# Optimization experiments

Measured on AMD Instinct MI355X. Metric: run time of the kernel, lower is better.

Reference implementation:

```python
import jax, jax.numpy as jnp
import numpy as np

DIM = 2048
N_HEADS = 16
Q_LORA = 1536
KV_LORA = 512
NOPE = 128
ROPE = 64
QK_HD = NOPE + ROPE  # 192
V_HD = 128
BS, SEQ = 2, 2048
EPS = 1e-6


def rmsnorm(x, w):
    var = jnp.mean(jnp.square(x), axis=-1, keepdims=True)
    return x * jax.lax.rsqrt(var + EPS) * w


def rope_cos_sin(seq_len, dim, dtype):
    inv_freq = 1.0 / (10000.0 ** (jnp.arange(0, dim, 2, dtype=jnp.float32) / dim))
    t = jnp.arange(seq_len, dtype=jnp.float32)
    freqs = jnp.outer(t, inv_freq)            # [S, dim/2]
    emb = jnp.concatenate([freqs, freqs], -1)  # [S, dim]
    return jnp.cos(emb).astype(dtype), jnp.sin(emb).astype(dtype)


def rotate_half(x):
    x1, x2 = jnp.split(x, 2, axis=-1)
    return jnp.concatenate([-x2, x1], axis=-1)


def apply_rope(x, cos, sin):
    # x: [B, S, H, D]; cos/sin: [S, D] -> broadcast over B, H
    return x * cos[None, :, None, :] + rotate_half(x) * sin[None, :, None, :]


def setup_inputs() -> dict:
    key = jax.random.key(0)
    ks = jax.random.split(key, 8)
    s = 0.02
    return {
        "x": jax.random.normal(ks[0], (BS, SEQ, DIM), jnp.float32),
        "wq_a_w": jax.random.normal(ks[1], (Q_LORA, DIM), jnp.float32) * s,
        "wq_a_b": jnp.zeros((Q_LORA,), jnp.float32),
        "q_norm_w": jnp.ones((Q_LORA,), jnp.float32),
        "wq_b_w": jax.random.normal(ks[2], (N_HEADS * QK_HD, Q_LORA), jnp.float32) * s,
        "wq_b_b": jnp.zeros((N_HEADS * QK_HD,), jnp.float32),
        "wkv_a_w": jax.random.normal(ks[3], (KV_LORA + ROPE, DIM), jnp.float32) * s,
        "wkv_a_b": jnp.zeros((KV_LORA + ROPE,), jnp.float32),
        "kv_norm_w": jnp.ones((KV_LORA,), jnp.float32),
        "wkv_b_w": jax.random.normal(ks[4], (N_HEADS * (NOPE + V_HD), KV_LORA), jnp.float32) * s,
        "wkv_b_b": jnp.zeros((N_HEADS * (NOPE + V_HD),), jnp.float32),
        "wo_w": jax.random.normal(ks[5], (DIM, N_HEADS * V_HD), jnp.float32) * s,
        "wo_b": jnp.zeros((DIM,), jnp.float32),
    }


def reference(x, wq_a_w, wq_a_b, q_norm_w, wq_b_w, wq_b_b,
              wkv_a_w, wkv_a_b, kv_norm_w, wkv_b_w, wkv_b_b, wo_w, wo_b):
    bs, seq_len, _ = x.shape
    # Q path: low-rank down, RMSNorm, up
    q = x @ wq_a_w.T + wq_a_b
    q = rmsnorm(q, q_norm_w)
    q = q @ wq_b_w.T + wq_b_b
    q = q.reshape(bs, seq_len, N_HEADS, QK_HD)
    q_nope, q_pe = q[..., :NOPE], q[..., NOPE:]
    # KV path: joint low-rank + decoupled rope key
    kv = x @ wkv_a_w.T + wkv_a_b
    kv_c, k_pe = kv[..., :KV_LORA], kv[..., KV_LORA:]
    k_pe = k_pe[:, :, None, :]  # [B, S, 1, ROPE]
    cos, sin = rope_cos_sin(seq_len, ROPE, x.dtype)
    q_pe = apply_rope(q_pe, cos, sin)
    k_pe = apply_rope(k_pe, cos, sin)
    # naive mode: materialize per-head K/V
    kv_c = rmsnorm(kv_c, kv_norm_w)
    kvb = (kv_c @ wkv_b_w.T + wkv_b_b).reshape(bs, seq_len, N_HEADS, NOPE + V_HD)
    k_nope, v = kvb[..., :NOPE], kvb[..., NOPE:]
    q_full = jnp.concatenate([q_nope, q_pe], axis=-1)            # [B,S,H,192]
    k_full = jnp.concatenate(
        [k_nope, jnp.broadcast_to(k_pe, (bs, seq_len, N_HEADS, ROPE))], axis=-1)
    scale = 1.0 / np.sqrt(QK_HD)
    scores = jnp.einsum('bqhd,bkhd->bhqk', q_full, k_full) * scale
    causal = jnp.tril(jnp.ones((seq_len, seq_len), bool))
    scores = jnp.where(causal[None, None], scores, jnp.finfo(scores.dtype).min)
    attn = jax.nn.softmax(scores, axis=-1)
    out = jnp.einsum('bhqk,bkhd->bqhd', attn, v)
    out = out.reshape(bs, seq_len, N_HEADS * V_HD)
    return out @ wo_w.T + wo_b
```

## Files before the change

kernel.cpp:

```cpp
#include <hip/hip_runtime.h>

#define SEQ 2048
#define NHEADS 16

typedef __bf16 bf16;
typedef __bf16 bf16x8 __attribute__((ext_vector_type(8)));
typedef __bf16 bf16x4v __attribute__((ext_vector_type(4)));
typedef float f32x4 __attribute__((ext_vector_type(4)));
typedef unsigned short u16x4 __attribute__((ext_vector_type(4)));
typedef unsigned short u16x8 __attribute__((ext_vector_type(8)));

static __device__ __forceinline__ float bf2f(unsigned short u) {
    union { unsigned u32; float f; } v; v.u32 = ((unsigned)u) << 16; return v.f;
}
static __device__ __forceinline__ unsigned short f2bf(float f) {
    union { float f; unsigned u; } v; v.f = f;
    unsigned u = v.u;
    unsigned r = u + 0x7fffu + ((u >> 16) & 1u);
    return (unsigned short)(r >> 16);
}

static __device__ __forceinline__ void g2l16(const unsigned short* g, unsigned short* l) {
    __builtin_amdgcn_global_load_lds(
        (const __attribute__((address_space(1))) unsigned int*)(unsigned long long)g,
        (__attribute__((address_space(3))) unsigned int*)(unsigned int)(unsigned long long)l,
        16, 0, 0);
}

__global__ void detect_dtype(const unsigned* __restrict__ qnw, int* __restrict__ flag) {
    if (threadIdx.x == 0 && blockIdx.x == 0)
        *flag = (qnw[0] == 0x3F800000u) ? 1 : 0;
}

struct CvtArgs {
    const void* src[13];
    unsigned short* dst[13];
    int n[13];
    int startblk[14];
};
__global__ __launch_bounds__(256) void to_bf16_all(CvtArgs a, const int* __restrict__ flag) {
    int bx = blockIdx.x;
    int t = 0;
    while (bx >= a.startblk[t + 1]) ++t;
    int base = (bx - a.startblk[t]) * 4096;
    int n = a.n[t];
    int hi = base + 4096; if (hi > n) hi = n;
    int cnt = hi - base;
    if (*flag) {
        const f32x4* s = (const f32x4*)a.src[t] + (base >> 2);
        u16x4* d = (u16x4*)(a.dst[t] + base);
        int c4 = cnt >> 2;
        for (int e = threadIdx.x; e < c4; e += 256) {
            f32x4 v = s[e];
            u16x4 o;
#pragma unroll
            for (int j = 0; j < 4; ++j) o[j] = f2bf(v[j]);
            d[e] = o;
        }
    } else {
        const uint4* s = (const uint4*)a.src[t] + (base >> 3);
        uint4* d = (uint4*)(a.dst[t] + base);
        int c8 = cnt >> 3;
        for (int e = threadIdx.x; e < c8; e += 256) d[e] = s[e];
    }
}

struct GemmP {
    const unsigned short* A; int lda;
    const unsigned short* W;
    const unsigned short* bias;
    unsigned short* C; float* Cf; int ldc;
    int N; int K; const int* flagp;
    int nbx;
    float oscale;
};

static __device__ void gemm_body(const GemmP g, int bx, int by,
                                 unsigned short* Al, unsigned short* Bl)
{
    const int lane = threadIdx.x & 63;
    const int w    = threadIdx.x >> 6;
    const int r    = lane & 15;
    const int quad = lane >> 4;
    const int m0 = by << 7;
    const int n0 = bx << 7;
    const int wr = (w >> 1) << 6;
    const int wc = (w & 1) << 6;

    const int srow = lane >> 2;
    const int scol = (lane & 3) << 3;
    const int j0 = w * 2, j1 = w * 2 + 1;

    const unsigned short* a0 = g.A + (size_t)(m0 + j0 * 16 + srow) * g.lda + scol;
    const unsigned short* a1 = g.A + (size_t)(m0 + j1 * 16 + srow) * g.lda + scol;
    int bn0 = n0 + j0 * 16 + srow; if (bn0 >= g.N) bn0 = g.N - 1;
    int bn1 = n0 + j1 * 16 + srow; if (bn1 >= g.N) bn1 = g.N - 1;
    const unsigned short* b0 = g.W + (size_t)bn0 * g.K + scol;
    const unsigned short* b1 = g.W + (size_t)bn1 * g.K + scol;

    f32x4 acc[4][4];
#pragma unroll
    for (int mt = 0; mt < 4; ++mt)
#pragma unroll
        for (int nt = 0; nt < 4; ++nt) acc[mt][nt] = (f32x4){0.f, 0.f, 0.f, 0.f};

    auto stage = [&](int buf, int kb) {
        unsigned short* Ad = Al + (buf << 12);
        unsigned short* Bd = Bl + (buf << 12);
        g2l16(a0 + kb, &Ad[j0 * 512 + lane * 8]);
        g2l16(a1 + kb, &Ad[j1 * 512 + lane * 8]);
        g2l16(b0 + kb, &Bd[j0 * 512 + lane * 8]);
        g2l16(b1 + kb, &Bd[j1 * 512 + lane * 8]);
    };

    stage(0, 0);
    __syncthreads();
    int cur = 0;
    for (int kb = 0; kb < g.K; kb += 32) {
        if (kb + 32 < g.K) stage(cur ^ 1, kb + 32);

        const unsigned short* As = Al + (cur << 12);
        const unsigned short* Bs = Bl + (cur << 12);
        bf16x8 af[4], bfr[4];
#pragma unroll
        for (int mt = 0; mt < 4; ++mt)
            af[mt] = *(const bf16x8*)&As[(wr + mt * 16 + r) * 32 + quad * 8];
#pragma unroll
        for (int nt = 0; nt < 4; ++nt)
            bfr[nt] = *(const bf16x8*)&Bs[(wc + nt * 16 + r) * 32 + quad * 8];
#pragma unroll
        for (int mt = 0; mt < 4; ++mt)
#pragma unroll
            for (int nt = 0; nt < 4; ++nt)
                acc[mt][nt] = __builtin_amdgcn_mfma_f32_16x16x32_bf16(af[mt], bfr[nt], acc[mt][nt], 0, 0, 0);

        __syncthreads();
        cur ^= 1;
    }

    int outf = (g.Cf && g.flagp) ? *g.flagp : 0;
    float bv[4];
#pragma unroll
    for (int nt = 0; nt < 4; ++nt) {
        int col = n0 + wc + nt * 16 + r;
        bv[nt] = (g.bias && col < g.N) ? bf2f(g.bias[col]) : 0.f;
    }
#pragma unroll
    for (int mt = 0; mt < 4; ++mt) {
#pragma unroll
        for (int i = 0; i < 4; ++i) {
            int row = m0 + wr + mt * 16 + quad * 4 + i;
#pragma unroll
            for (int nt = 0; nt < 4; ++nt) {
                int col = n0 + wc + nt * 16 + r;
                if (col < g.N) {
                    float v = (acc[mt][nt][i] + bv[nt]) * g.oscale;
                    size_t idx = (size_t)row * g.ldc + col;
                    if (g.Cf) {
                        if (outf) g.Cf[idx] = v;
                        else      ((unsigned short*)g.Cf)[idx] = f2bf(v);
                    } else {
                        g.C[idx] = f2bf(v);
                    }
                }
            }
        }
    }
}

__global__ __launch_bounds__(256) void gemm_one(GemmP g) {
    __shared__ unsigned short Al[2 * 4096];
    __shared__ unsigned short Bl[2 * 4096];
    gemm_body(g, blockIdx.x, blockIdx.y, Al, Bl);
}

__global__ __launch_bounds__(256) void gemm_two(GemmP g0, GemmP g1, int nblk0) {
    __shared__ unsigned short Al[2 * 4096];
    __shared__ unsigned short Bl[2 * 4096];
    int id = blockIdx.x;
    if (id < nblk0) {
        gemm_body(g0, id % g0.nbx, id / g0.nbx, Al, Bl);
    } else {
        id -= nblk0;
        gemm_body(g1, id % g1.nbx, id / g1.nbx, Al, Bl);
    }
}

__global__ __launch_bounds__(256) void rmsnorm_ip2(
    unsigned short* __restrict__ d0, int s0w, int w0w, const unsigned short* __restrict__ w0,
    unsigned short* __restrict__ d1, int s1w, int w1w, const unsigned short* __restrict__ w1,
    int rows0)
{
    __shared__ float red[256];
    int row = blockIdx.x;
    unsigned short* p; const unsigned short* wt; int stride, width;
    if (row < rows0) { p = d0; wt = w0; stride = s0w; width = w0w; }
    else { row -= rows0; p = d1; wt = w1; stride = s1w; width = w1w; }
    p += (size_t)row * stride;

    const int nv = width >> 3;
    u16x8* pv = (u16x8*)p;
    const u16x8* wv = (const u16x8*)wt;

    float ss = 0.f;
    for (int j = threadIdx.x; j < nv; j += 256) {
        u16x8 v = pv[j];
#pragma unroll
        for (int k = 0; k < 8; ++k) { float f = bf2f(v[k]); ss += f * f; }
    }
    red[threadIdx.x] = ss;
    __syncthreads();
    for (int s = 128; s > 0; s >>= 1) {
        if ((int)threadIdx.x < s) red[threadIdx.x] += red[threadIdx.x + s];
        __syncthreads();
    }
    float rstd = rsqrtf(red[0] / (float)width + 1e-6f);
    for (int j = threadIdx.x; j < nv; j += 256) {
        u16x8 v = pv[j], g = wv[j], o;
#pragma unroll
        for (int k = 0; k < 8; ++k) o[k] = f2bf(bf2f(v[k]) * rstd * bf2f(g[k]));
        pv[j] = o;
    }
}

__global__ __launch_bounds__(256) void rope_ip_all(
    unsigned short* __restrict__ qbuf, unsigned short* __restrict__ kvbf)
{
    __shared__ float cst[32], snt[32];
    int row = blockIdx.x;
    int s = row & (SEQ - 1);
    if (threadIdx.x < 32) {
        int i = threadIdx.x;
        float inv = exp2f(-(float)i * (13.2877123795f / 32.0f));
        float ang = (float)s * inv;
        cst[i] = cosf(ang); snt[i] = sinf(ang);
    }
    __syncthreads();
    for (int t = threadIdx.x; t < 544; t += 256) {
        int i = t & 31;
        float c = cst[i], sn = snt[i];
        unsigned short* p;
        if (t < 512) p = qbuf + (size_t)row * 3072 + (t >> 5) * 192 + 128;
        else         p = kvbf + (size_t)row * 576 + 512;
        float x1 = bf2f(p[i]), x2 = bf2f(p[i + 32]);
        p[i]      = f2bf(x1 * c - x2 * sn);
        p[i + 32] = f2bf(x2 * c + x1 * sn);
    }
}

__global__ __launch_bounds__(256) void mla_attn_mfma(
    const unsigned short* __restrict__ qbuf,
    const unsigned short* __restrict__ kvb,
    const unsigned short* __restrict__ kvbuf,
    unsigned short* __restrict__ attn_out)
{
    __shared__ unsigned short Kt[2][32 * 200];
    __shared__ unsigned short Vt[2][128 * 40];
    __shared__ unsigned short Pm[4][16 * 40];

    const int id    = blockIdx.x;
    const int bh    = (id & 7) + (((id >> 3) & 3) << 3);
    const int qtblk = id >> 5;
    const int b = bh >> 4, h = bh & 15;
    const int tid  = threadIdx.x;
    const int lane = tid & 63;
    const int w    = tid >> 6;
    const int r    = lane & 15;
    const int quad = lane >> 4;
    const int rowk0 = b * SEQ;

    int kldso[3];
    const unsigned short* ksrc[3];
    int krst[3];
#pragma unroll
    for (int j = 0; j < 3; ++j) {
        int v = tid + j * 256;
        int row = v / 24, c = v % 24;
        kldso[j] = row * 200 + c * 8;
        if (c < 16) { ksrc[j] = kvb + (size_t)(rowk0 + row) * 4096 + h * 256 + c * 8; krst[j] = 4096; }
        else        { ksrc[j] = kvbuf + (size_t)(rowk0 + row) * 576 + 512 + (c - 16) * 8; krst[j] = 576; }
    }
    const int vp  = tid & 15;
    const int vdc = tid >> 4;
    const unsigned short* vsrc = kvb + (size_t)(rowk0 + 2 * vp) * 4096 + h * 256 + 128 + vdc * 8;

    auto stageK = [&](int buf, const uint4& k0, const uint4& k1, const uint4& k2) {
        *(uint4*)&Kt[buf][kldso[0]] = k0;
        *(uint4*)&Kt[buf][kldso[1]] = k1;
        *(uint4*)&Kt[buf][kldso[2]] = k2;
    };
    auto stageV = [&](int buf, const uint4& va, const uint4& vb_) {
        const unsigned* ea = (const unsigned*)&va;
        const unsigned* eb = (const unsigned*)&vb_;
        unsigned short* Vd = &Vt[buf][0];
#pragma unroll
        for (int t = 0; t < 4; ++t) {
            unsigned pe = (ea[t] & 0xffffu) | (eb[t] << 16);
            unsigned po = (ea[t] >> 16) | (eb[t] & 0xffff0000u);
            *(unsigned*)&Vd[(vdc * 8 + 2 * t) * 40 + 2 * vp]     = pe;
            *(unsigned*)&Vd[(vdc * 8 + 2 * t + 1) * 40 + 2 * vp] = po;
        }
    };

    unsigned short* Pw = Pm[w];

#pragma unroll 1
    for (int half = 0; half < 2; ++half) {
        const int qt = half ? (31 - qtblk) : qtblk;
        const int qbase = qt * 64 + w * 16;
        const int nkb = 2 * qt + 2;
        const int itmax = 2 * qt + (w >> 1);

        bf16x8 qf[6];
        {
            const unsigned short* qp =
                qbuf + (size_t)(rowk0 + qbase + r) * 3072 + h * 192 + quad * 8;
#pragma unroll
            for (int t = 0; t < 6; ++t) qf[t] = *(const bf16x8*)(qp + t * 32);
        }

        f32x4 O[8];
#pragma unroll
        for (int f = 0; f < 8; ++f) O[f] = (f32x4){0.f, 0.f, 0.f, 0.f};
        float mi = -1e30f, li = 0.f;

        uint4 pk0, pk1, pk2, pv0, pv1;

        __syncthreads();
        pk0 = *(const uint4*)(ksrc[0]);
        pk1 = *(const uint4*)(ksrc[1]);
        pk2 = *(const uint4*)(ksrc[2]);
        pv0 = *(const uint4*)(vsrc);
        pv1 = *(const uint4*)(vsrc + 4096);
        stageK(0, pk0, pk1, pk2);
        stageV(0, pv0, pv1);
        __syncthreads();

#pragma unroll 1
        for (int it = 0; it < nkb; ++it) {
            const int p = it & 1;
            const int kb = it * 32;
            const bool more = (it + 1 < nkb);

            if (more) {
                const size_t koff = (size_t)(kb + 32);
                pk0 = *(const uint4*)(ksrc[0] + koff * krst[0]);
                pk1 = *(const uint4*)(ksrc[1] + koff * krst[1]);
                pk2 = *(const uint4*)(ksrc[2] + koff * krst[2]);
                pv0 = *(const uint4*)(vsrc + koff * 4096);
                pv1 = *(const uint4*)(vsrc + koff * 4096 + 4096);
            }

            if (it <= itmax) {
                f32x4 s0 = {0.f, 0.f, 0.f, 0.f}, s1 = {0.f, 0.f, 0.f, 0.f};
                __builtin_amdgcn_s_setprio(1);
#pragma unroll
                for (int t = 0; t < 6; ++t) {
                    bf16x8 k0 = *(const bf16x8*)&Kt[p][r * 200 + t * 32 + quad * 8];
                    bf16x8 k1 = *(const bf16x8*)&Kt[p][(16 + r) * 200 + t * 32 + quad * 8];
                    s0 = __builtin_amdgcn_mfma_f32_16x16x32_bf16(k0, qf[t], s0, 0, 0, 0);
                    s1 = __builtin_amdgcn_mfma_f32_16x16x32_bf16(k1, qf[t], s1, 0, 0, 0);
                }
                __builtin_amdgcn_s_setprio(0);

                const int qrow = qbase + r;
                float a0[4], a1[4];
                float mx = -1e30f;
                if (kb + 31 > qbase) {
#pragma unroll
                    for (int i = 0; i < 4; ++i) {
                        a0[i] = (kb + quad * 4 + i      <= qrow) ? s0[i] : -1e30f;
                        a1[i] = (kb + 16 + quad * 4 + i <= qrow) ? s1[i] : -1e30f;
                        mx = fmaxf(mx, fmaxf(a0[i], a1[i]));
                    }
                } else {
#pragma unroll
                    for (int i = 0; i < 4; ++i) {
                        a0[i] = s0[i];
                        a1[i] = s1[i];
                        mx = fmaxf(mx, fmaxf(a0[i], a1[i]));
                    }
                }
                mx = fmaxf(mx, __shfl_xor(mx, 16, 64));
                mx = fmaxf(mx, __shfl_xor(mx, 32, 64));

                if (!__all(mx <= mi + 8.f)) {
                    float mn = fmaxf(mi, mx);
                    float al = __builtin_amdgcn_exp2f(mi - mn);
#pragma unroll
                    for (int f = 0; f < 8; ++f) O[f] *= al;
                    li *= al;
                    mi = mn;
                }

                float p0[4], p1[4], ps = 0.f;
#pragma unroll
                for (int i = 0; i < 4; ++i) {
                    p0[i] = __builtin_amdgcn_exp2f(a0[i] - mi);
                    p1[i] = __builtin_amdgcn_exp2f(a1[i] - mi);
                    ps += p0[i] + p1[i];
                }
                ps += __shfl_xor(ps, 16, 64);
                ps += __shfl_xor(ps, 32, 64);
                li += ps;

                bf16x4v b0v, b1v;
#pragma unroll
                for (int i = 0; i < 4; ++i) {
                    b0v[i] = (__bf16)p0[i];
                    b1v[i] = (__bf16)p1[i];
                }
                *(bf16x4v*)&Pw[r * 40 + quad * 4]      = b0v;
                *(bf16x4v*)&Pw[r * 40 + 16 + quad * 4] = b1v;

                bf16x8 pf = *(const bf16x8*)&Pw[r * 40 + quad * 8];
                __builtin_amdgcn_s_setprio(1);
#pragma unroll
                for (int f = 0; f < 8; ++f) {
                    bf16x8 vb = *(const bf16x8*)&Vt[p][(f * 16 + r) * 40 + quad * 8];
                    O[f] = __builtin_amdgcn_mfma_f32_16x16x32_bf16(vb, pf, O[f], 0, 0, 0);
                }
                __builtin_amdgcn_s_setprio(0);
            }

            if (more) {
                const int q2 = 1 - p;
                stageK(q2, pk0, pk1, pk2);
                stageV(q2, pv0, pv1);
                __syncthreads();
            }
        }

        float inv = (li > 0.f) ? (1.f / li) : 0.f;
        unsigned short* orow = attn_out + (size_t)(rowk0 + qbase + r) * 2048 + h * 128;
#pragma unroll
        for (int f = 0; f < 8; ++f) {
            bf16x4v o;
#pragma unroll
            for (int i = 0; i < 4; ++i) o[i] = (__bf16)(O[f][i] * inv);
            *(bf16x4v*)&orow[f * 16 + quad * 4] = o;
        }
    }
}

extern "C" void kernel_launch(void* const* d_in, const int* in_sizes, int n_in,
                              void* d_out, int out_size, void* d_ws, size_t ws_size,
                              hipStream_t stream)
{
    char* ws = (char*)d_ws;
    size_t off = 0;
    auto alloc = [&](size_t bytes) -> void* {
        void* p = ws + off;
        off = (off + bytes + 255) & ~(size_t)255;
        return p;
    };

    int* flag = (int*)alloc(256);

    const int nx = 4096 * 2048;
    unsigned short* xb    = (unsigned short*)alloc((size_t)nx * 2);
    unsigned short* wqa   = (unsigned short*)alloc((size_t)1536 * 2048 * 2);
    unsigned short* wqab  = (unsigned short*)alloc(1536 * 2);
    unsigned short* qnw   = (unsigned short*)alloc(1536 * 2);
    unsigned short* wqb   = (unsigned short*)alloc((size_t)3072 * 1536 * 2);
    unsigned short* wqbb  = (unsigned short*)alloc(3072 * 2);
    unsigned short* wkva  = (unsigned short*)alloc((size_t)576 * 2048 * 2);
    unsigned short* wkvab = (unsigned short*)alloc(576 * 2);
    unsigned short* kvnw  = (unsigned short*)alloc(512 * 2);
    unsigned short* wkvb  = (unsigned short*)alloc((size_t)4096 * 512 * 2);
    unsigned short* wkvbb = (unsigned short*)alloc(4096 * 2);
    unsigned short* wo    = (unsigned short*)alloc((size_t)2048 * 2048 * 2);
    unsigned short* wob   = (unsigned short*)alloc(2048 * 2);

    unsigned short* qa   = (unsigned short*)alloc((size_t)4096 * 1536 * 2);
    unsigned short* qbuf = (unsigned short*)alloc((size_t)4096 * 3072 * 2);
    unsigned short* kvbf = (unsigned short*)alloc((size_t)4096 * 576 * 2);
    unsigned short* kvb  = (unsigned short*)alloc((size_t)4096 * 4096 * 2);
    unsigned short* attn = xb;

    const int M = 4096;
    dim3 blk(256);

    detect_dtype<<<dim3(1), dim3(64), 0, stream>>>((const unsigned*)d_in[3], flag);

    {
        CvtArgs a;
        unsigned short* dsts[13] = {xb, wqa, wqab, qnw, wqb, wqbb, wkva, wkvab, kvnw, wkvb, wkvbb, wo, wob};
        int pb = 0;
        for (int i = 0; i < 13; ++i) {
            a.src[i] = d_in[i];
            a.dst[i] = dsts[i];
            a.n[i] = in_sizes[i];
            a.startblk[i] = pb;
            pb += (in_sizes[i] + 4095) / 4096;
        }
        a.startblk[13] = pb;
        to_bf16_all<<<dim3(pb), blk, 0, stream>>>(a, flag);
    }

    auto mkg = [](const unsigned short* A, int lda, const unsigned short* W,
                  const unsigned short* bias, unsigned short* C, float* Cf, int ldc,
                  int N, int K, const int* fl, float osc) -> GemmP {
        GemmP g;
        g.A = A; g.lda = lda; g.W = W; g.bias = bias;
        g.C = C; g.Cf = Cf; g.ldc = ldc; g.N = N; g.K = K; g.flagp = fl;
        g.nbx = (N + 127) / 128;
        g.oscale = osc;
        return g;
    };

    {
        GemmP gqa  = mkg(xb, 2048, wqa,  wqab,  qa,   nullptr, 1536, 1536, 2048, nullptr, 1.f);
        GemmP gkva = mkg(xb, 2048, wkva, wkvab, kvbf, nullptr, 576,  576,  2048, nullptr, 1.f);
        int nb0 = gqa.nbx * (M / 128), nb1 = gkva.nbx * (M / 128);
        gemm_two<<<dim3(nb0 + nb1), blk, 0, stream>>>(gqa, gkva, nb0);
    }

    rmsnorm_ip2<<<dim3(2 * M), blk, 0, stream>>>(qa, 1536, 1536, qnw,
                                                 kvbf, 576, 512, kvnw, M);

    {
        GemmP gqb  = mkg(qa,   1536, wqb,  wqbb,  qbuf, nullptr, 3072, 3072, 1536, nullptr, 0.1041175648f);
        GemmP gkvb = mkg(kvbf, 576,  wkvb, wkvbb, kvb,  nullptr, 4096, 4096, 512,  nullptr, 1.f);
        int nb0 = gqb.nbx * (M / 128), nb1 = gkvb.nbx * (M / 128);
        gemm_two<<<dim3(nb0 + nb1), blk, 0, stream>>>(gqb, gkvb, nb0);
    }

    rope_ip_all<<<dim3(M), blk, 0, stream>>>(qbuf, kvbf);

    mla_attn_mfma<<<dim3(512), blk, 0, stream>>>(qbuf, kvb, kvbf, attn);

    {
        GemmP gout = mkg(attn, 2048, wo, wob, nullptr, (float*)d_out, 2048, 2048, 2048, flag, 1.f);
        gemm_one<<<dim3(gout.nbx, M / 128), blk, 0, stream>>>(gout);
    }
}
```

Baseline: 447.0 us.

## Switch attention to 32x32x16 MFMA with 128-row query tiles per block

The attention kernel now has each wave handle 32 query rows using 32x32x16 bf16 MFMA for both QK^T and PV, so each block covers a 128-row query tile. This replaces the old scheme of 16-row waves on 16x16x32 MFMA that processed two mirrored 64-row tiles per block. Each K/V tile loaded into LDS is now reused across more query rows, and fewer MFMA issues and shuffles are needed per score tile. In exchange, accumulator registers grow (12 Q fragments plus four 16-wide accumulators), which may lower occupancy. The block-to-tile mapping for causal load balance also changes, and it must agree with the grid size set in the unseen host code.

```diff
diff --git a/kernel.cpp b/kernel.cpp
--- a/kernel.cpp
+++ b/kernel.cpp
@@ -7,6 +7,7 @@
 typedef __bf16 bf16x8 __attribute__((ext_vector_type(8)));
 typedef __bf16 bf16x4v __attribute__((ext_vector_type(4)));
 typedef float f32x4 __attribute__((ext_vector_type(4)));
+typedef float f32x16 __attribute__((ext_vector_type(16)));
 typedef unsigned short u16x4 __attribute__((ext_vector_type(4)));
 typedef unsigned short u16x8 __attribute__((ext_vector_type(8)));
 
@@ -256,17 +257,18 @@
 {
     __shared__ unsigned short Kt[2][32 * 200];
     __shared__ unsigned short Vt[2][128 * 40];
-    __shared__ unsigned short Pm[4][16 * 40];
-
-    const int id    = blockIdx.x;
-    const int bh    = (id & 7) + (((id >> 3) & 3) << 3);
-    const int qtblk = id >> 5;
+    __shared__ unsigned short Pm[4][32 * 40];
+
+    const int id  = blockIdx.x;
+    const int bh  = (id & 7) + (((id >> 3) & 3) << 3);
+    const int hi5 = id >> 5;
+    const int t   = (hi5 < 8) ? hi5 : 23 - hi5;
     const int b = bh >> 4, h = bh & 15;
     const int tid  = threadIdx.x;
     const int lane = tid & 63;
     const int w    = tid >> 6;
-    const int r    = lane & 15;
-    const int quad = lane >> 4;
+    const int l31  = lane & 31;
+    const int hi   = lane >> 5;
     const int rowk0 = b * SEQ;
 
     int kldso[3];
@@ -294,153 +296,149 @@
         const unsigned* eb = (const unsigned*)&vb_;
         unsigned short* Vd = &Vt[buf][0];
 #pragma unroll
-        for (int t = 0; t < 4; ++t) {
-            unsigned pe = (ea[t] & 0xffffu) | (eb[t] << 16);
-            unsigned po = (ea[t] >> 16) | (eb[t] & 0xffff0000u);
-            *(unsigned*)&Vd[(vdc * 8 + 2 * t) * 40 + 2 * vp]     = pe;
-            *(unsigned*)&Vd[(vdc * 8 + 2 * t + 1) * 40 + 2 * vp] = po;
+        for (int tt = 0; tt < 4; ++tt) {
+            unsigned pe = (ea[tt] & 0xffffu) | (eb[tt] << 16);
+            unsigned po = (ea[tt] >> 16) | (eb[tt] & 0xffff0000u);
+            *(unsigned*)&Vd[(vdc * 8 + 2 * tt) * 40 + 2 * vp]     = pe;
+            *(unsigned*)&Vd[(vdc * 8 + 2 * tt + 1) * 40 + 2 * vp] = po;
         }
     };
 
     unsigned short* Pw = Pm[w];
 
+    const int qbase = t * 128 + w * 32;
+    const int qrow  = qbase + l31;
+    const int nkb   = 4 * t + 4;
+    const int itmaxw = 4 * t + w;
+
+    bf16x8 qf[12];
+    {
+        const unsigned short* qp =
+            qbuf + (size_t)(rowk0 + qrow) * 3072 + h * 192 + hi * 8;
+#pragma unroll
+        for (int kt = 0; kt < 12; ++kt) qf[kt] = *(const bf16x8*)(qp + kt * 16);
+    }
+
+    f32x16 O[4];
+#pragma unroll
+    for (int d = 0; d < 4; ++d)
+#pragma unroll
+        for (int i = 0; i < 16; ++i) O[d][i] = 0.f;
+    float mi = -1e30f, li = 0.f;
+
+    uint4 pk0, pk1, pk2, pv0, pv1;
+
+    pk0 = *(const uint4*)(ksrc[0]);
+    pk1 = *(const uint4*)(ksrc[1]);
+    pk2 = *(const uint4*)(ksrc[2]);
+    pv0 = *(const uint4*)(vsrc);
+    pv1 = *(const uint4*)(vsrc + 4096);
+    stageK(0, pk0, pk1, pk2);
+    stageV(0, pv0, pv1);
+    __syncthreads();
+
 #pragma unroll 1
-    for (int half = 0; half < 2; ++half) {
-        const int qt = half ? (31 - qtblk) : qtblk;
-        const int qbase = qt * 64 + w * 16;
-        const int nkb = 2 * qt + 2;
-        const int itmax = 2 * qt + (w >> 1);
-
-        bf16x8 qf[6];
-        {
-            const unsigned short* qp =
-                qbuf + (size_t)(rowk0 + qbase + r) * 3072 + h * 192 + quad * 8;
-#pragma unroll
-            for (int t = 0; t < 6; ++t) qf[t] = *(const bf16x8*)(qp + t * 32);
-        }
-
-        f32x4 O[8];
-#pragma unroll
-        for (int f = 0; f < 8; ++f) O[f] = (f32x4){0.f, 0.f, 0.f, 0.f};
-        float mi = -1e30f, li = 0.f;
-
-        uint4 pk0, pk1, pk2, pv0, pv1;
-
-        __syncthreads();
-        pk0 = *(const uint4*)(ksrc[0]);
-        pk1 = *(const uint4*)(ksrc[1]);
-        pk2 = *(const uint4*)(ksrc[2]);
-        pv0 = *(const uint4*)(vsrc);
-        pv1 = *(const uint4*)(vsrc + 4096);
-        stageK(0, pk0, pk1, pk2);
-        stageV(0, pv0, pv1);
-        __syncthreads();
-
-#pragma unroll 1
-        for (int it = 0; it < nkb; ++it) {
-            const int p = it & 1;
-            const int kb = it * 32;
-            const bool more = (it + 1 < nkb);
-
-            if (more) {
-                const size_t koff = (size_t)(kb + 32);
-                pk0 = *(const uint4*)(ksrc[0] + koff * krst[0]);
-                pk1 = *(const uint4*)(ksrc[1] + koff * krst[1]);
-                pk2 = *(const uint4*)(ksrc[2] + koff * krst[2]);
-                pv0 = *(const uint4*)(vsrc + koff * 4096);
-                pv1 = *(const uint4*)(vsrc + koff * 4096 + 4096);
-            }
-
-            if (it <= itmax) {
-                f32x4 s0 = {0.f, 0.f, 0.f, 0.f}, s1 = {0.f, 0.f, 0.f, 0.f};
-                __builtin_amdgcn_s_setprio(1);
-#pragma unroll
-                for (int t = 0; t < 6; ++t) {
-                    bf16x8 k0 = *(const bf16x8*)&Kt[p][r * 200 + t * 32 + quad * 8];
-                    bf16x8 k1 = *(const bf16x8*)&Kt[p][(16 + r) * 200 + t * 32 + quad * 8];
-                    s0 = __builtin_amdgcn_mfma_f32_16x16x32_bf16(k0, qf[t], s0, 0, 0, 0);
-                    s1 = __builtin_amdgcn_mfma_f32_16x16x32_bf16(k1, qf[t], s1, 0, 0, 0);
+    for (int it = 0; it < nkb; ++it) {
+        const int p = it & 1;
+        const int kb = it * 32;
+        const bool more = (it + 1 < nkb);
+
+        if (more) {
+            const size_t koff = (size_t)(kb + 32);
+            pk0 = *(const uint4*)(ksrc[0] + koff * krst[0]);
+            pk1 = *(const uint4*)(ksrc[1] + koff * krst[1]);
+            pk2 = *(const uint4*)(ksrc[2] + koff * krst[2]);
+            pv0 = *(const uint4*)(vsrc + koff * 4096);
+            pv1 = *(const uint4*)(vsrc + koff * 4096 + 4096);
+        }
+
+        if (it <= itmaxw) {
+            f32x16 S;
+#pragma unroll
+            for (int i = 0; i < 16; ++i) S[i] = 0.f;
+            __builtin_amdgcn_s_setprio(1);
+#pragma unroll
+            for (int kt = 0; kt < 12; ++kt) {
+                bf16x8 kf = *(const bf16x8*)&Kt[p][l31 * 200 + kt * 16 + hi * 8];
+                S = __builtin_amdgcn_mfma_f32_32x32x16_bf16(kf, qf[kt], S, 0, 0, 0);
+            }
+            __builtin_amdgcn_s_setprio(0);
+
+            float a[16];
+            float mx = -1e30f;
+            if (kb + 31 > qbase) {
+#pragma unroll
+                for (int i = 0; i < 16; ++i) {
+                    int key = kb + (i & 3) + 8 * (i >> 2) + 4 * hi;
+                    a[i] = (key <= qrow) ? S[i] : -1e30f;
+                    mx = fmaxf(mx, a[i]);
                 }
-                __builtin_amdgcn_s_setprio(0);
-
-                const int qrow = qbase + r;
-                float a0[4], a1[4];
-                float mx = -1e30f;
-                if (kb + 31 > qbase) {
-#pragma unroll
-                    for (int i = 0; i < 4; ++i) {
-                        a0[i] = (kb + quad * 4 + i      <= qrow) ? s0[i] : -1e30f;
-                        a1[i] = (kb + 16 + quad * 4 + i <= qrow) ? s1[i] : -1e30f;
-                        mx = fmaxf(mx, fmaxf(a0[i], a1[i]));
-                    }
-                } else {
-#pragma unroll
-                    for (int i = 0; i < 4; ++i) {
-                        a0[i] = s0[i];
-                        a1[i] = s1[i];
-                        mx = fmaxf(mx, fmaxf(a0[i], a1[i]));
-                    }
-                }
-                mx = fmaxf(mx, __shfl_xor(mx, 16, 64));
-                mx = fmaxf(mx, __shfl_xor(mx, 32, 64));
-
-                if (!__all(mx <= mi + 8.f)) {
-                    float mn = fmaxf(mi, mx);
-                    float al = __builtin_amdgcn_exp2f(mi - mn);
-#pragma unroll
-                    for (int f = 0; f < 8; ++f) O[f] *= al;
-                    li *= al;
-                    mi = mn;
-                }
-
-                float p0[4], p1[4], ps = 0.f;
-#pragma unroll
-                for (int i = 0; i < 4; ++i) {
-                    p0[i] = __builtin_amdgcn_exp2f(a0[i] - mi);
-                    p1[i] = __builtin_amdgcn_exp2f(a1[i] - mi);
-                    ps += p0[i] + p1[i];
-                }
-                ps += __shfl_xor(ps, 16, 64);
-                ps += __shfl_xor(ps, 32, 64);
-                li += ps;
-
-                bf16x4v b0v, b1v;
-#pragma unroll
-                for (int i = 0; i < 4; ++i) {
-                    b0v[i] = (__bf16)p0[i];
-                    b1v[i] = (__bf16)p1[i];
-                }
-                *(bf16x4v*)&Pw[r * 40 + quad * 4]      = b0v;
-                *(bf16x4v*)&Pw[r * 40 + 16 + quad * 4] = b1v;
-
-                bf16x8 pf = *(const bf16x8*)&Pw[r * 40 + quad * 8];
-                __builtin_amdgcn_s_setprio(1);
-#pragma unroll
-                for (int f = 0; f < 8; ++f) {
-                    bf16x8 vb = *(const bf16x8*)&Vt[p][(f * 16 + r) * 40 + quad * 8];
-                    O[f] = __builtin_amdgcn_mfma_f32_16x16x32_bf16(vb, pf, O[f], 0, 0, 0);
-                }
-                __builtin_amdgcn_s_setprio(0);
-            }
-
-            if (more) {
-                const int q2 = 1 - p;
-                stageK(q2, pk0, pk1, pk2);
-                stageV(q2, pv0, pv1);
-                __syncthreads();
-            }
-        }
-
-        float inv = (li > 0.f) ? (1.f / li) : 0.f;
-        unsigned short* orow = attn_out + (size_t)(rowk0 + qbase + r) * 2048 + h * 128;
-#pragma unroll
-        for (int f = 0; f < 8; ++f) {
+            } else {
+#pragma unroll
+                for (int i = 0; i < 16; ++i) { a[i] = S[i]; mx = fmaxf(mx, a[i]); }
+            }
+            mx = fmaxf(mx, __shfl_xor(mx, 32, 64));
+
+            if (!__all(mx <= mi + 8.f)) {
+                float mn = fmaxf(mi, mx);
+                float al = __builtin_amdgcn_exp2f(mi - mn);
+#pragma unroll
+                for (int d = 0; d < 4; ++d)
+#pragma unroll
+                    for (int i = 0; i < 16; ++i) O[d][i] *= al;
+                li *= al;
+                mi = mn;
+            }
+
+            float pr[16], ps = 0.f;
+#pragma unroll
+            for (int i = 0; i < 16; ++i) {
+                pr[i] = __builtin_amdgcn_exp2f(a[i] - mi);
+                ps += pr[i];
+            }
+            ps += __shfl_xor(ps, 32, 64);
+            li += ps;
+
+#pragma unroll
+            for (int g2 = 0; g2 < 4; ++g2) {
+                bf16x4v p4;
+#pragma unroll
+                for (int i = 0; i < 4; ++i) p4[i] = (__bf16)pr[g2 * 4 + i];
+                *(bf16x4v*)&Pw[l31 * 40 + g2 * 8 + 4 * hi] = p4;
+            }
+
+            bf16x8 pb0 = *(const bf16x8*)&Pw[l31 * 40 + hi * 8];
+            bf16x8 pb1 = *(const bf16x8*)&Pw[l31 * 40 + 16 + hi * 8];
+            __builtin_amdgcn_s_setprio(1);
+#pragma unroll
+            for (int d = 0; d < 4; ++d) {
+                bf16x8 v0 = *(const bf16x8*)&Vt[p][(d * 32 + l31) * 40 + hi * 8];
+                bf16x8 v1 = *(const bf16x8*)&Vt[p][(d * 32 + l31) * 40 + 16 + hi * 8];
+                O[d] = __builtin_amdgcn_mfma_f32_32x32x16_bf16(v0, pb0, O[d], 0, 0, 0);
+                O[d] = __builtin_amdgcn_mfma_f32_32x32x16_bf16(v1, pb1, O[d], 0, 0, 0);
+            }
+            __builtin_amdgcn_s_setprio(0);
+        }
+
+        if (more) {
+            const int q2 = 1 - p;
+            stageK(q2, pk0, pk1, pk2);
+            stageV(q2, pv0, pv1);
+            __syncthreads();
+        }
+    }
+
+    float inv = (li > 0.f) ? (1.f / li) : 0.f;
+    unsigned short* orow = attn_out + (size_t)(rowk0 + qrow) * 2048 + h * 128;
+#pragma unroll
+    for (int d = 0; d < 4; ++d)
+#pragma unroll
+        for (int g2 = 0; g2 < 4; ++g2) {
             bf16x4v o;
 #pragma unroll
-            for (int i = 0; i < 4; ++i) o[i] = (__bf16)(O[f][i] * inv);
-            *(bf16x4v*)&orow[f * 16 + quad * 4] = o;
-        }
-    }
+            for (int i = 0; i < 4; ++i) o[i] = (__bf16)(O[d][g2 * 4 + i] * inv);
+            *(bf16x4v*)&orow[d * 32 + g2 * 8 + 4 * hi] = o;
+        }
 }
 
 extern "C" void kernel_launch(void* const* d_in, const int* in_sizes, int n_in,
```

New measurement: 454.1 us. Within noise of the previous version (+1.6%).
